# Kernel tuning notes

Hardware: AMD Instinct MI355X
Metric: run time of the kernel (lower is better)

## Reference

```python
import jax, jax.numpy as jnp
import numpy as np

V, D, N, E, H = 80000, 300, 32, 64, 4
C = D // H          # per-head out channels (concat -> D)
B, T, U, L = 32, 35, 1024, 3
VG = 50000          # last_idx_globals - last_idx_senses
NEG_SLOPE = 0.2


def setup_inputs() -> dict:
    key = jax.random.key(0)
    ks = jax.random.split(key, 16)
    s = 0.02
    inp = {
        'x_indices': jax.random.randint(ks[0], (B, T, N), 0, V),
        'edge_index': jax.random.randint(ks[1], (B, T, 2, E), 0, N),
        'X': jax.random.normal(ks[2], (V, D), jnp.float32) * s,
        'gat_W': jax.random.normal(ks[3], (D, H * C), jnp.float32) * s,
        'att_src': jax.random.normal(ks[4], (H, C), jnp.float32) * s,
        'att_dst': jax.random.normal(ks[5], (H, C), jnp.float32) * s,
        'gat_bias': jnp.zeros((H * C,), jnp.float32),
        'W_ih0': jax.random.normal(ks[6], (4 * U, 2 * D), jnp.float32) * s,
        'W_ih_rest': jax.random.normal(ks[7], (L - 1, 4 * U, U), jnp.float32) * s,
        'W_hh': jax.random.normal(ks[8], (L, 4 * U, U), jnp.float32) * s,
        'b_ih': jnp.zeros((L, 4 * U), jnp.float32),
        'b_hh': jnp.zeros((L, 4 * U), jnp.float32),
        'lin_W': jax.random.normal(ks[9], (VG, U), jnp.float32) * s,
        'lin_b': jnp.zeros((VG,), jnp.float32),
    }
    return inp


def _gat_node0(X, x_indices, edge_index, gat_W, att_src, att_dst, gat_bias):
    # Batched GATConv over G = B*T tiny subgraphs of fixed size N; dense NxN
    # attention per subgraph is used since N=32 (G*H*N*N ~ 4.6M floats).
    b, t, n = x_indices.shape
    G = b * t
    idx = x_indices.reshape(G, n)
    ei = edge_index.reshape(G, 2, -1)
    x = X[idx]                                   # [G,N,D] embedding gather
    h = (x @ gat_W).reshape(G, n, H, C)          # [G,N,H,C]
    a_s = jnp.einsum('gnhc,hc->gnh', h, att_src)
    a_d = jnp.einsum('gnhc,hc->gnh', h, att_dst)
    # e[g,h,i,j] = leaky_relu(a_dst_i + a_src_j)  (messages j -> i)
    e = a_d.transpose(0, 2, 1)[:, :, :, None] + a_s.transpose(0, 2, 1)[:, :, None, :]
    e = jax.nn.leaky_relu(e, NEG_SLOPE)
    src, dst = ei[:, 0], ei[:, 1]
    g_ar = jnp.arange(G)[:, None]
    adj = jnp.zeros((G, n, n), bool).at[g_ar, dst, src].set(True)
    diag = jnp.arange(n)
    adj = adj.at[:, diag, diag].set(True)        # PyG GATConv adds self-loops
    e = jnp.where(adj[:, None, :, :], e, jnp.float32(-1e9))
    alpha = jax.nn.softmax(e, axis=-1)           # softmax over source nodes j
    out = jnp.einsum('ghij,gjhc->gihc', alpha, h)
    node0 = out[:, 0].reshape(G, H * C) + gat_bias  # only node 0 is consumed
    return node0.reshape(b, t, H * C)


def _lstm_layer(xs, Wi, Wh, bi, bh):
    # xs: [T,B,in]; PyTorch gate order i,f,g,o
    bsz, u = xs.shape[1], Wh.shape[1]
    def step(carry, xt):
        hp, cp = carry
        g = xt @ Wi.T + hp @ Wh.T + (bi + bh)
        i_, f_, gg, o_ = jnp.split(g, 4, axis=-1)
        c = jax.nn.sigmoid(f_) * cp + jax.nn.sigmoid(i_) * jnp.tanh(gg)
        hh = jax.nn.sigmoid(o_) * jnp.tanh(c)
        return (hh, c), hh
    init = (jnp.zeros((bsz, u), xs.dtype), jnp.zeros((bsz, u), xs.dtype))
    _, ys = jax.lax.scan(step, init, xs)
    return ys


def reference(x_indices, edge_index, X, gat_W, att_src, att_dst, gat_bias,
              W_ih0, W_ih_rest, W_hh, b_ih, b_hh, lin_W, lin_b):
    b, t, n = x_indices.shape
    node0 = _gat_node0(X, x_indices, edge_index, gat_W, att_src, att_dst, gat_bias)
    curr_emb = X[x_indices[:, :, 0]]                       # [B,T,D]
    sig = jnp.concatenate([curr_emb, node0], axis=-1)      # [B,T,2D]
    seq = sig.transpose(1, 0, 2)                           # [T,B,2D]
    ys = _lstm_layer(seq, W_ih0, W_hh[0], b_ih[0], b_hh[0])
    for l in range(W_ih_rest.shape[0]):
        ys = _lstm_layer(ys, W_ih_rest[l], W_hh[l + 1], b_ih[l + 1], b_hh[l + 1])
    lstm_out = ys.transpose(1, 0, 2).reshape(b * t, -1)    # [B*T,U]
    logits = lstm_out @ lin_W.T + lin_b                    # [B*T,VG]
    return jax.nn.log_softmax(logits, axis=-1)
```

## Files before the change

### kernel.cpp

```cpp
#include <hip/hip_runtime.h>

#define DEV __device__ __forceinline__

typedef __attribute__((ext_vector_type(8))) short short8;
typedef __attribute__((ext_vector_type(4))) float f32x4;
typedef unsigned short u16;

constexpr int kV = 80000, kD = 300, kNN = 32, kEE = 64, kHH = 4, kCC = 75;
constexpr int kB = 32, kT = 35, kU = 1024, kVG = 50000;
constexpr int kG = kB * kT;
constexpr int kM = kG;

constexpr size_t alignup(size_t x) { return (x + 255) & ~size_t(255); }
constexpr size_t OFF_BAR   = 0;
constexpr size_t OFF_WSRC  = 1024;
constexpr size_t OFF_WDST  = alignup(OFF_WSRC + 1200 * 4);
constexpr size_t OFF_BIAS  = alignup(OFF_WDST + 1200 * 4);
constexpr size_t OFF_SIG   = alignup(OFF_BIAS + 3 * 4096 * 4);
constexpr size_t OFF_WX0   = alignup(OFF_SIG + (size_t)35 * 32 * 640 * 2);
constexpr size_t OFF_WX12  = alignup(OFF_WX0 + (size_t)4096 * 640 * 2);
constexpr size_t OFF_GATES = alignup(OFF_WX12 + (size_t)2 * 4096 * 1024 * 2);
constexpr size_t OFF_HIST  = alignup(OFF_GATES + (size_t)1120 * 4096 * 4);
constexpr size_t OFF_PART  = alignup(OFF_HIST + (size_t)3 * 35 * 32 * 1024 * 2);
constexpr size_t OFF_LSE   = alignup(OFF_PART + (size_t)1120 * 784 * 8);
constexpr size_t OFF_LINWB = alignup(OFF_LSE + 1120 * 4);
constexpr size_t kLinWBytes = (size_t)kVG * 1024 * 2;
constexpr size_t kNeedBW   = OFF_LINWB + kLinWBytes;
constexpr size_t OFF_WHB   = alignup(OFF_LINWB + kLinWBytes);
constexpr size_t kWhbBytes = (size_t)3 * 4096 * 1024 * 2;
constexpr size_t kNeedWHB  = OFF_WHB + kWhbBytes;

DEV u16 f2bf(float f) {
  union { float f; unsigned u; } v; v.f = f;
  unsigned r = v.u + 0x7fffu + ((v.u >> 16) & 1u);
  return (u16)(r >> 16);
}
DEV float fexp(float x) { return __builtin_amdgcn_exp2f(x * 1.4426950408889634f); }
DEV float fsigm(float x) {
  float t = __builtin_amdgcn_exp2f(-1.4426950408889634f * x);
  return __builtin_amdgcn_rcpf(1.f + t);
}
DEV float ftanh(float x) {
  float xc = fminf(fmaxf(x, -20.f), 20.f);
  float t = __builtin_amdgcn_exp2f(2.8853900817779268f * xc);
  return (t - 1.f) * __builtin_amdgcn_rcpf(t + 1.f);
}
DEV f32x4 mfma16(short8 a, short8 b, f32x4 c) {
  return __builtin_amdgcn_mfma_f32_16x16x32_bf16(a, b, c, 0, 0, 0);
}
DEV void store_u16_llc(u16* p, u16 v) {
  unsigned vv = v;
  asm volatile("global_store_short %0, %1, off sc0 sc1"
               :: "v"(p), "v"(vv) : "memory");
}
DEV void gll16(const void* g, void* l) {
  __builtin_amdgcn_global_load_lds(
      (const __attribute__((address_space(1))) unsigned int*)g,
      (__attribute__((address_space(3))) unsigned int*)l, 16, 0, 0);
}
DEV void conv_slice(const float* src, u16* dst, long n, long tid0, long stride) {
  long n8 = n >> 3;
  for (long i = tid0; i < n8; i += stride) {
    long o = i * 8;
    float4 a = *(const float4*)(src + o);
    float4 b = *(const float4*)(src + o + 4);
    u16 t[8] = {f2bf(a.x), f2bf(a.y), f2bf(a.z), f2bf(a.w),
                f2bf(b.x), f2bf(b.y), f2bf(b.z), f2bf(b.w)};
    *(uint4*)(dst + o) = *(const uint4*)t;
  }
}

__global__ void prep_small(const float* __restrict__ gat_W,
                           const float* __restrict__ att_src,
                           const float* __restrict__ att_dst,
                           const float* __restrict__ b_ih,
                           const float* __restrict__ b_hh,
                           float* __restrict__ ws_src, float* __restrict__ ws_dst,
                           float* __restrict__ bias_sum) {
  int total = 1200 + 1200 + 3 * 4096;
  for (int i = blockIdx.x * blockDim.x + threadIdx.x; i < total; i += gridDim.x * blockDim.x) {
    if (i < 1200) {
      int d = i >> 2, h = i & 3;
      float s = 0.f;
      for (int c = 0; c < kCC; ++c) s += gat_W[d * 300 + h * kCC + c] * att_src[h * kCC + c];
      ws_src[i] = s;
    } else if (i < 2400) {
      int j = i - 1200; int d = j >> 2, h = j & 3;
      float s = 0.f;
      for (int c = 0; c < kCC; ++c) s += gat_W[d * 300 + h * kCC + c] * att_dst[h * kCC + c];
      ws_dst[j] = s;
    } else {
      int j = i - 2400;
      bias_sum[j] = b_ih[j] + b_hh[j];
    }
  }
}

__global__ void wx_prep(const float* __restrict__ W_ih0,
                        const float* __restrict__ W_ih_rest,
                        const float* __restrict__ W_hh,
                        u16* __restrict__ wx0, u16* __restrict__ wx12,
                        u16* __restrict__ whb, int nhh_layers) {
  const int n0 = 4096 * 640;
  const int n12 = 2 * 4096 * 1024;
  const int nhh = nhh_layers * 4096 * 1024;
  int total = n0 + n12 + nhh;
  for (int i = blockIdx.x * blockDim.x + threadIdx.x; i < total; i += gridDim.x * blockDim.x) {
    if (i < n0) {
      int row = i / 640, col = i - row * 640;
      float v = (col < 600) ? W_ih0[row * 600 + col] : 0.f;
      wx0[i] = f2bf(v);
    } else if (i < n0 + n12) {
      int j = i - n0;
      wx12[j] = f2bf(W_ih_rest[j]);
    } else {
      int j = i - n0 - n12;
      if (whb) whb[j] = f2bf(W_hh[j]);
    }
  }
}

__global__ void wb_conv(const float* __restrict__ W, u16* __restrict__ Wb) {
  const long n = (long)kVG * 1024;
  conv_slice(W, Wb, n, (long)(blockIdx.x * blockDim.x + threadIdx.x),
             (long)gridDim.x * blockDim.x);
}

__global__ void __launch_bounds__(256) gat_kernel(
    const int* __restrict__ x_indices, const int* __restrict__ edge_index,
    const float* __restrict__ X, const float* __restrict__ gat_W,
    const float* __restrict__ gat_bias, const float* __restrict__ ws_src,
    const float* __restrict__ ws_dst, u16* __restrict__ sig) {
  __shared__ float xs[32][301];
  __shared__ float a_s[32][4];
  __shared__ float a_d0[4];
  __shared__ float alpha[4][32];
  __shared__ float xw[4][301];
  __shared__ int allowed[32];
  int g = blockIdx.x, tid = threadIdx.x;
  const int* idx = x_indices + g * 32;
  for (int i = tid; i < 32 * 300; i += 256) {
    int j = i / 300, d2 = i - j * 300;
    xs[j][d2] = X[(size_t)idx[j] * 300 + d2];
  }
  if (tid < 32) allowed[tid] = (tid == 0) ? 1 : 0;
  __syncthreads();
  if (tid < 128) {
    int j = tid >> 2, h = tid & 3;
    float s = 0.f;
    for (int d2 = 0; d2 < 300; ++d2) s += xs[j][d2] * ws_src[d2 * 4 + h];
    a_s[j][h] = s;
  } else if (tid < 132) {
    int h = tid - 128; float s = 0.f;
    for (int d2 = 0; d2 < 300; ++d2) s += xs[0][d2] * ws_dst[d2 * 4 + h];
    a_d0[h] = s;
  } else if (tid >= 192) {
    int e = tid - 192;
    int src = edge_index[g * 128 + e];
    int dst = edge_index[g * 128 + 64 + e];
    if (dst == 0) allowed[src] = 1;
  }
  __syncthreads();
  if (tid < 4) {
    int h = tid;
    float ev[32];
    float mx = -1e30f;
    #pragma unroll
    for (int j = 0; j < 32; ++j) {
      float v = a_d0[h] + a_s[j][h];
      v = (v > 0.f) ? v : 0.2f * v;
      v = allowed[j] ? v : -1e9f;
      ev[j] = v; mx = fmaxf(mx, v);
    }
    float ssum = 0.f;
    #pragma unroll
    for (int j = 0; j < 32; ++j) { float p = fexp(ev[j] - mx); ev[j] = p; ssum += p; }
    float inv = 1.f / ssum;
    #pragma unroll
    for (int j = 0; j < 32; ++j) alpha[h][j] = ev[j] * inv;
  }
  __syncthreads();
  for (int i = tid; i < 4 * 300; i += 256) {
    int h = i / 300, d2 = i - h * 300;
    float s = 0.f;
    #pragma unroll
    for (int j = 0; j < 32; ++j) s += alpha[h][j] * xs[j][d2];
    xw[h][d2] = s;
  }
  __syncthreads();
  int t = g % 35, b = g / 35;
  u16* srow = sig + ((size_t)t * 32 + b) * 640;
  for (int hc = tid; hc < 300; hc += 256) {
    srow[hc] = f2bf(xs[0][hc]);
    int h = hc / 75;
    float s = gat_bias[hc];
    for (int d2 = 0; d2 < 300; ++d2) s += xw[h][d2] * gat_W[d2 * 300 + hc];
    srow[300 + hc] = f2bf(s);
  }
  for (int i2 = 600 + tid; i2 < 640; i2 += 256) srow[i2] = 0;
}

__global__ void __launch_bounds__(256, 4) gemm_ig(
    const u16* __restrict__ A, const u16* __restrict__ Bw,
    float* __restrict__ gates, int K) {
  int bid = blockIdx.x;
  int bm = bid % 9, bn = bid / 9;
  int m0 = bm * 128, n0 = bn * 128;
  int tid = threadIdx.x, w = tid >> 6, lane = tid & 63, l15 = lane & 15, lhi = lane >> 4;
  int wm = w & 1, wn = w >> 1;
  __shared__ u16 As[2][128][32];
  __shared__ u16 Bs[2][128][32];
  int cl = ((lane & 3) ^ ((lane >> 3) & 3)) * 8;
  int am0 = m0 + w * 32 + (lane >> 2);
  int am1 = am0 + 16;
  const u16* arow0 = A + (size_t)((am0 < kM) ? am0 : 0) * K + cl;
  const u16* arow1 = A + (size_t)((am1 < kM) ? am1 : 0) * K + cl;
  int bn0r = n0 + w * 32 + (lane >> 2);
  const u16* brow0 = Bw + (size_t)bn0r * K + cl;
  const u16* brow1 = Bw + (size_t)(bn0r + 16) * K + cl;
  const int koff = (lhi ^ ((l15 >> 1) & 3)) * 8;

  f32x4 acc[4][4];
  #pragma unroll
  for (int i = 0; i < 4; ++i)
    #pragma unroll
    for (int j = 0; j < 4; ++j) { f32x4 z = {0.f, 0.f, 0.f, 0.f}; acc[i][j] = z; }

  auto ISSUE = [&](int k0, int buf) {
    gll16(arow0 + k0, &As[buf][w * 32][0]);
    gll16(arow1 + k0, &As[buf][w * 32 + 16][0]);
    gll16(brow0 + k0, &Bs[buf][w * 32][0]);
    gll16(brow1 + k0, &Bs[buf][w * 32 + 16][0]);
  };
  int nkt = K >> 5;
  ISSUE(0, 0);
  for (int kt = 0; kt < nkt; ++kt) {
    int cur = kt & 1;
    if (kt < nkt - 1) {
      ISSUE((kt + 1) * 32, cur ^ 1);
      asm volatile("s_waitcnt vmcnt(4)" ::: "memory");
    } else {
      asm volatile("s_waitcnt vmcnt(0)" ::: "memory");
    }
    __builtin_amdgcn_s_barrier();
    __builtin_amdgcn_sched_barrier(0);
    short8 bfr[4];
    #pragma unroll
    for (int nt = 0; nt < 4; ++nt)
      bfr[nt] = *(const short8*)&Bs[cur][wn * 64 + nt * 16 + l15][koff];
    #pragma unroll
    for (int mt = 0; mt < 4; ++mt) {
      short8 af = *(const short8*)&As[cur][wm * 64 + mt * 16 + l15][koff];
      #pragma unroll
      for (int nt = 0; nt < 4; ++nt)
        acc[mt][nt] = mfma16(af, bfr[nt], acc[mt][nt]);
    }
    __builtin_amdgcn_sched_barrier(0);
    __builtin_amdgcn_s_barrier();
  }
  #pragma unroll
  for (int mt = 0; mt < 4; ++mt) {
    #pragma unroll
    for (int r = 0; r < 4; ++r) {
      int m = m0 + wm * 64 + mt * 16 + lhi * 4 + r;
      if (m < kM) {
        float* orow = gates + (size_t)m * 4096;
        #pragma unroll
        for (int nt = 0; nt < 4; ++nt) {
          int n = n0 + wn * 64 + nt * 16 + l15;
          orow[(n & 1023) * 4 + (n >> 10)] = acc[mt][nt][r];
        }
      }
    }
  }
}

__global__ void __launch_bounds__(256, 1) lstm_rec(
    const float* __restrict__ W_hh_l,
    const u16* __restrict__ whb_l,
    const float* __restrict__ gates,
    const float* __restrict__ bias_l,
    u16* __restrict__ hout,
    unsigned* flags, unsigned sbase,
    const float* csrcA, u16* cdstA, long ncA,
    const float* csrcB, u16* cdstB, long ncB) {
  if (blockIdx.x >= 128) {
    long tid0 = (long)(blockIdx.x - 128) * 256 + threadIdx.x;
    long stride = 128L * 256;
    if (cdstA) conv_slice(csrcA, cdstA, ncA, tid0, stride);
    if (cdstB) conv_slice(csrcB, cdstB, ncB, tid0, stride);
    return;
  }
  const int p = blockIdx.x;
  const int tid = threadIdx.x;
  const int w = tid >> 6, lane = tid & 63, l15 = lane & 15, lhi = lane >> 4;
  __shared__ u16 whs[32][1032];
  __shared__ float pred[4][32][33];
  if (whb_l) {
    for (int i = tid; i < 32 * 128; i += 256) {
      int row = i >> 7, seg = i & 127;
      int g = row >> 3, jj = row & 7;
      uint4 v = *(const uint4*)(whb_l + (((size_t)(g * 1024 + p * 8 + jj)) << 10) + seg * 8);
      *(uint4*)&whs[row][seg * 8] = v;
    }
  } else {
    for (int i = tid; i < 32 * 256; i += 256) {
      int row = i >> 8, seg = i & 255;
      int g = row >> 3, jj = row & 7;
      const float* src = W_hh_l + (((size_t)(g * 1024 + p * 8 + jj)) << 10) + seg * 4;
      float4 f = *(const float4*)src;
      u16 tmp[4] = {f2bf(f.x), f2bf(f.y), f2bf(f.z), f2bf(f.w)};
      *(uint2*)&whs[row][seg * 4] = *(const uint2*)tmp;
    }
  }
  const int bb = tid >> 3, jj2 = tid & 7;
  float bias_r[4];
  #pragma unroll
  for (int g = 0; g < 4; ++g) bias_r[g] = bias_l[g * 1024 + p * 8 + jj2];
  float c_reg = 0.f;
  const int kbase = w * 256;
  const float4* gb4 = (const float4*)gates + (size_t)bb * 1024 + (p * 8 + jj2);
  const unsigned* myflags = flags + w * 32 + (lane & 31);

  float4 gx = gb4[0];

  for (int t = 0; t < 35; ++t) {
    float4 gxn;
    if (t > 0) {
      unsigned tgt = sbase + (unsigned)t;
      while (!__all((int)(__hip_atomic_load(myflags, __ATOMIC_RELAXED,
                                            __HIP_MEMORY_SCOPE_AGENT) >= tgt)))
        __builtin_amdgcn_s_sleep(1);
      asm volatile("" ::: "memory");
      const u16* hp = hout + (size_t)(t - 1) * 32 * 1024;
      const u16* hrow0 = hp + l15 * 1024 + lhi * 8;
      const u16* hrow1 = hp + (l15 + 16) * 1024 + lhi * 8;
      f32x4 acc00 = {0,0,0,0}, acc01 = {0,0,0,0}, acc10 = {0,0,0,0}, acc11 = {0,0,0,0};
      #pragma unroll
      for (int kk = 0; kk < 8; ++kk) {
        int k = kbase + kk * 32;
        short8 bf0 = *(const short8*)(hrow0 + k);
        short8 bf1 = *(const short8*)(hrow1 + k);
        short8 af0 = *(const short8*)&whs[l15][k + lhi * 8];
        short8 af1 = *(const short8*)&whs[16 + l15][k + lhi * 8];
        acc00 = mfma16(af0, bf0, acc00);
        acc01 = mfma16(af0, bf1, acc01);
        acc10 = mfma16(af1, bf0, acc10);
        acc11 = mfma16(af1, bf1, acc11);
      }
      if (t < 34) gxn = gb4[(size_t)(t + 1) * 32768];
      #pragma unroll
      for (int r = 0; r < 4; ++r) {
        pred[w][lhi * 4 + r][l15]       = acc00[r];
        pred[w][lhi * 4 + r][l15 + 16]  = acc01[r];
        pred[w][16 + lhi * 4 + r][l15]      = acc10[r];
        pred[w][16 + lhi * 4 + r][l15 + 16] = acc11[r];
      }
      __syncthreads();
    } else {
      gxn = gb4[(size_t)32 * 1024];
    }
    float pre[4];
    #pragma unroll
    for (int g = 0; g < 4; ++g) {
      float s = 0.f;
      if (t > 0) {
        int row = g * 8 + jj2;
        s = pred[0][row][bb] + pred[1][row][bb] + pred[2][row][bb] + pred[3][row][bb];
      }
      pre[g] = s;
    }
    float iv = gx.x + pre[0] + bias_r[0];
    float fv = gx.y + pre[1] + bias_r[1];
    float gv = gx.z + pre[2] + bias_r[2];
    float ov = gx.w + pre[3] + bias_r[3];
    float cc = fsigm(fv) * c_reg + fsigm(iv) * ftanh(gv);
    float hh = fsigm(ov) * ftanh(cc);
    c_reg = cc;
    store_u16_llc(hout + ((size_t)(t * 32 + bb)) * 1024 + p * 8 + jj2, f2bf(hh));
    __syncthreads();
    if (t < 34 && tid == 0)
      __hip_atomic_store(flags + p, sbase + (unsigned)t + 1u,
                         __ATOMIC_RELAXED, __HIP_MEMORY_SCOPE_AGENT);
    gx = gxn;
  }
}

DEV void logits_epilogue(f32x4 (&acc)[4][4], int m0, int n0, int wm, int wn,
                         int l15, int lhi, const float* lin_b,
                         float* out, float2* partials, int bn) {
  float bcol[4]; int ncol[4];
  #pragma unroll
  for (int nt = 0; nt < 4; ++nt) {
    int n = n0 + wn * 64 + nt * 16 + l15;
    ncol[nt] = n;
    bcol[nt] = (n < kVG) ? lin_b[n] : -INFINITY;
  }
  #pragma unroll
  for (int mt = 0; mt < 4; ++mt) {
    #pragma unroll
    for (int r = 0; r < 4; ++r) {
      int m = m0 + wm * 64 + mt * 16 + lhi * 4 + r;
      float v0 = acc[mt][0][r] + bcol[0];
      float v1 = acc[mt][1][r] + bcol[1];
      float v2 = acc[mt][2][r] + bcol[2];
      float v3 = acc[mt][3][r] + bcol[3];
      bool mok = (m < kM);
      if (mok) {
        float* orow = out + (size_t)m * kVG;
        if (ncol[0] < kVG) orow[ncol[0]] = v0;
        if (ncol[1] < kVG) orow[ncol[1]] = v1;
        if (ncol[2] < kVG) orow[ncol[2]] = v2;
        if (ncol[3] < kVG) orow[ncol[3]] = v3;
      }
      float mx = fmaxf(fmaxf(v0, v1), fmaxf(v2, v3));
      #pragma unroll
      for (int d2 = 1; d2 < 16; d2 <<= 1) mx = fmaxf(mx, __shfl_xor(mx, d2, 64));
      float sv = 0.f;
      sv += (v0 > -1e30f) ? fexp(v0 - mx) : 0.f;
      sv += (v1 > -1e30f) ? fexp(v1 - mx) : 0.f;
      sv += (v2 > -1e30f) ? fexp(v2 - mx) : 0.f;
      sv += (v3 > -1e30f) ? fexp(v3 - mx) : 0.f;
      #pragma unroll
      for (int d2 = 1; d2 < 16; d2 <<= 1) sv += __shfl_xor(sv, d2, 64);
      if (mok && l15 == 0)
        partials[(size_t)m * 784 + bn * 2 + wn] = make_float2(mx, sv);
    }
  }
}

__global__ void __launch_bounds__(256, 4) gemm_logits_async(
    const u16* __restrict__ hist2, const u16* __restrict__ linwb,
    const float* __restrict__ lin_b, float* __restrict__ out,
    float2* __restrict__ partials) {
  int nwg = gridDim.x, orig = blockIdx.x;
  int q = nwg >> 3, r = nwg & 7, xcd = orig & 7, off = orig >> 3;
  int bid = (xcd < r ? xcd * (q + 1) : r * (q + 1) + (xcd - r) * q) + off;
  int bm = bid % 9, bn = bid / 9;
  int m0 = bm * 128, n0 = bn * 128;
  int tid = threadIdx.x, w = tid >> 6, lane = tid & 63, l15 = lane & 15, lhi = lane >> 4;
  int wm = w & 1, wn = w >> 1;
  __shared__ u16 As[2][128][32];
  __shared__ u16 Bs[2][128][32];
  int cl = ((lane & 3) ^ ((lane >> 3) & 3)) * 8;
  int am0 = m0 + w * 32 + (lane >> 2);
  int am1 = am0 + 16;
  int mm0 = (am0 < kM) ? am0 : 0, mm1 = (am1 < kM) ? am1 : 0;
  const u16* arow0 = hist2 + (((size_t)((mm0 % 35) * 32 + mm0 / 35)) << 10) + cl;
  const u16* arow1 = hist2 + (((size_t)((mm1 % 35) * 32 + mm1 / 35)) << 10) + cl;
  int nr0 = n0 + w * 32 + (lane >> 2);
  int nn0 = (nr0 < kVG) ? nr0 : 0, nn1 = (nr0 + 16 < kVG) ? nr0 + 16 : 0;
  const u16* brow0 = linwb + ((size_t)nn0 << 10) + cl;
  const u16* brow1 = linwb + ((size_t)nn1 << 10) + cl;
  const int koff = (lhi ^ ((l15 >> 1) & 3)) * 8;

  f32x4 acc[4][4];
  #pragma unroll
  for (int i = 0; i < 4; ++i)
    #pragma unroll
    for (int j = 0; j < 4; ++j) { f32x4 z = {0.f, 0.f, 0.f, 0.f}; acc[i][j] = z; }

  auto ISSUE = [&](int k0, int buf) {
    gll16(arow0 + k0, &As[buf][w * 32][0]);
    gll16(arow1 + k0, &As[buf][w * 32 + 16][0]);
    gll16(brow0 + k0, &Bs[buf][w * 32][0]);
    gll16(brow1 + k0, &Bs[buf][w * 32 + 16][0]);
  };
  ISSUE(0, 0);
  for (int kt = 0; kt < 32; ++kt) {
    int cur = kt & 1;
    if (kt < 31) {
      ISSUE((kt + 1) * 32, cur ^ 1);
      asm volatile("s_waitcnt vmcnt(4)" ::: "memory");
    } else {
      asm volatile("s_waitcnt vmcnt(0)" ::: "memory");
    }
    __builtin_amdgcn_s_barrier();
    __builtin_amdgcn_sched_barrier(0);
    short8 bfr[4];
    #pragma unroll
    for (int nt = 0; nt < 4; ++nt)
      bfr[nt] = *(const short8*)&Bs[cur][wn * 64 + nt * 16 + l15][koff];
    #pragma unroll
    for (int mt = 0; mt < 4; ++mt) {
      short8 af = *(const short8*)&As[cur][wm * 64 + mt * 16 + l15][koff];
      #pragma unroll
      for (int nt = 0; nt < 4; ++nt)
        acc[mt][nt] = mfma16(af, bfr[nt], acc[mt][nt]);
    }
    __builtin_amdgcn_sched_barrier(0);
    __builtin_amdgcn_s_barrier();
  }
  logits_epilogue(acc, m0, n0, wm, wn, l15, lhi, lin_b, out, partials, bn);
}

__global__ void __launch_bounds__(256, 1) gemm_logits_fb(
    const u16* __restrict__ hist2, const float* __restrict__ lin_W,
    const float* __restrict__ lin_b, float* __restrict__ out,
    float2* __restrict__ partials) {
  int nwg = gridDim.x, orig = blockIdx.x;
  int q = nwg >> 3, r = nwg & 7, xcd = orig & 7, off = orig >> 3;
  int bid = (xcd < r ? xcd * (q + 1) : r * (q + 1) + (xcd - r) * q) + off;
  int bm = bid % 9, bn = bid / 9;
  int m0 = bm * 128, n0 = bn * 128;
  int tid = threadIdx.x, w = tid >> 6, lane = tid & 63, l15 = lane & 15, lhi = lane >> 4;
  int wm = w & 1, wn = w >> 1;
  __shared__ u16 As[128][40];
  __shared__ u16 Bs[128][40];
  f32x4 acc[4][4];
  #pragma unroll
  for (int i = 0; i < 4; ++i)
    #pragma unroll
    for (int j = 0; j < 4; ++j) { f32x4 z = {0.f, 0.f, 0.f, 0.f}; acc[i][j] = z; }
  for (int kt = 0; kt < 32; ++kt) {
    int k0 = kt * 32;
    #pragma unroll
    for (int q2 = 0; q2 < 2; ++q2) {
      int c = tid * 2 + q2; int row = c >> 2; int ch = c & 3;
      int m = m0 + row;
      uint4 av{0u, 0u, 0u, 0u};
      if (m < kM) {
        int b = m / 35; int t = m - b * 35;
        av = *(const uint4*)(hist2 + ((size_t)(t * 32 + b) << 10) + k0 + ch * 8);
      }
      *(uint4*)&As[row][ch * 8] = av;
      int n = n0 + row;
      uint4 bv{0u, 0u, 0u, 0u};
      if (n < kVG) {
        const float* src = lin_W + (size_t)n * 1024 + k0 + ch * 8;
        float4 f0 = *(const float4*)(src);
        float4 f1 = *(const float4*)(src + 4);
        bv.x = (unsigned)f2bf(f0.x) | ((unsigned)f2bf(f0.y) << 16);
        bv.y = (unsigned)f2bf(f0.z) | ((unsigned)f2bf(f0.w) << 16);
        bv.z = (unsigned)f2bf(f1.x) | ((unsigned)f2bf(f1.y) << 16);
        bv.w = (unsigned)f2bf(f1.z) | ((unsigned)f2bf(f1.w) << 16);
      }
      *(uint4*)&Bs[row][ch * 8] = bv;
    }
    __syncthreads();
    short8 bfr[4];
    #pragma unroll
    for (int nt = 0; nt < 4; ++nt)
      bfr[nt] = *(const short8*)&Bs[wn * 64 + nt * 16 + l15][lhi * 8];
    #pragma unroll
    for (int mt = 0; mt < 4; ++mt) {
      short8 af = *(const short8*)&As[wm * 64 + mt * 16 + l15][lhi * 8];
      #pragma unroll
      for (int nt = 0; nt < 4; ++nt)
        acc[mt][nt] = mfma16(af, bfr[nt], acc[mt][nt]);
    }
    __syncthreads();
  }
  logits_epilogue(acc, m0, n0, wm, wn, l15, lhi, lin_b, out, partials, bn);
}

__global__ void reduce_rows(const float2* __restrict__ partials, float* __restrict__ lse) {
  int m = blockIdx.x, tid = threadIdx.x;
  float mx = -INFINITY, s = 0.f;
  for (int j = tid; j < 782; j += 256) {
    float2 p = partials[(size_t)m * 784 + j];
    if (p.x > mx) { s = s * fexp(mx - p.x) + p.y; mx = p.x; }
    else          { s += p.y * fexp(p.x - mx); }
  }
  for (int d = 1; d < 64; d <<= 1) {
    float omx = __shfl_xor(mx, d, 64);
    float os  = __shfl_xor(s, d, 64);
    if (omx > mx) { s = s * fexp(mx - omx) + os; mx = omx; }
    else          { s += os * fexp(omx - mx); }
  }
  __shared__ float smx[4], ssum[4];
  int w = tid >> 6;
  if ((tid & 63) == 0) { smx[w] = mx; ssum[w] = s; }
  __syncthreads();
  if (tid == 0) {
    for (int i = 1; i < 4; ++i) {
      float omx = smx[i], os = ssum[i];
      if (omx > mx) { s = s * fexp(mx - omx) + os; mx = omx; }
      else          { s += os * fexp(omx - mx); }
    }
    lse[m] = mx + logf(s);
  }
}

__global__ void sub_lse(float* __restrict__ out, const float* __restrict__ lse) {
  const int total4 = 14000000;
  for (int i = blockIdx.x * blockDim.x + threadIdx.x; i < total4; i += gridDim.x * blockDim.x) {
    int m = i / 12500;
    float4 v = ((float4*)out)[i];
    float L = lse[m];
    v.x -= L; v.y -= L; v.z -= L; v.w -= L;
    ((float4*)out)[i] = v;
  }
}

extern "C" void kernel_launch(void* const* d_in, const int* in_sizes, int n_in,
                              void* d_out, int out_size, void* d_ws, size_t ws_size,
                              hipStream_t stream) {
  const int*   x_indices  = (const int*)d_in[0];
  const int*   edge_index = (const int*)d_in[1];
  const float* X          = (const float*)d_in[2];
  const float* gat_W      = (const float*)d_in[3];
  const float* att_src    = (const float*)d_in[4];
  const float* att_dst    = (const float*)d_in[5];
  const float* gat_bias   = (const float*)d_in[6];
  const float* W_ih0      = (const float*)d_in[7];
  const float* W_ih_rest  = (const float*)d_in[8];
  const float* W_hh       = (const float*)d_in[9];
  const float* b_ih       = (const float*)d_in[10];
  const float* b_hh       = (const float*)d_in[11];
  const float* lin_W      = (const float*)d_in[12];
  const float* lin_b      = (const float*)d_in[13];
  float* out = (float*)d_out;
  char* ws = (char*)d_ws;

  unsigned* flags    = (unsigned*)(ws + OFF_BAR);
  float*    ws_src   = (float*)(ws + OFF_WSRC);
  float*    ws_dst   = (float*)(ws + OFF_WDST);
  float*    bias_sum = (float*)(ws + OFF_BIAS);
  u16*      sig      = (u16*)(ws + OFF_SIG);
  u16*      wx0      = (u16*)(ws + OFF_WX0);
  u16*      wx12     = (u16*)(ws + OFF_WX12);
  float*    gates    = (float*)(ws + OFF_GATES);
  u16*      hist     = (u16*)(ws + OFF_HIST);
  float2*   partials = (float2*)(ws + OFF_PART);
  float*    lse      = (float*)(ws + OFF_LSE);
  u16*      linwb    = (u16*)(ws + OFF_LINWB);
  u16*      whb      = (u16*)(ws + OFF_WHB);
  bool use_bw  = (ws_size >= kNeedBW);
  bool use_whb = (ws_size >= kNeedWHB);
  bool hide = use_bw && use_whb;

  u16* hist0 = hist;
  u16* hist1 = hist + (size_t)35 * 32 * 1024;
  u16* hist2 = hist + (size_t)2 * 35 * 32 * 1024;
  const long nLinHalf = (long)kVG * 1024 / 2;

  hipMemsetAsync(ws + OFF_BAR, 0, 1024, stream);
  prep_small<<<64, 256, 0, stream>>>(gat_W, att_src, att_dst, b_ih, b_hh,
                                     ws_src, ws_dst, bias_sum);
  wx_prep<<<2048, 256, 0, stream>>>(W_ih0, W_ih_rest, W_hh, wx0, wx12,
                                    use_whb ? whb : nullptr, hide ? 1 : 3);
  if (use_bw && !hide) wb_conv<<<2048, 256, 0, stream>>>(lin_W, linwb);
  gat_kernel<<<kG, 256, 0, stream>>>(x_indices, edge_index, X, gat_W, gat_bias,
                                     ws_src, ws_dst, sig);
  gemm_ig<<<288, 256, 0, stream>>>(sig, wx0, gates, 640);
  lstm_rec<<<hide ? 256 : 128, 256, 0, stream>>>(
      W_hh, use_whb ? whb : nullptr, gates, bias_sum, hist0, flags, 0u,
      hide ? W_hh + (size_t)4096 * 1024 : nullptr,
      hide ? whb + (size_t)4096 * 1024 : nullptr, (long)2 * 4096 * 1024,
      hide ? lin_W : nullptr, hide ? linwb : nullptr, nLinHalf);
  gemm_ig<<<288, 256, 0, stream>>>(hist0, wx12, gates, 1024);
  lstm_rec<<<hide ? 256 : 128, 256, 0, stream>>>(
      W_hh + (size_t)4096 * 1024,
      use_whb ? whb + (size_t)4096 * 1024 : nullptr,
      gates, bias_sum + 4096, hist1, flags, 34u,
      hide ? lin_W + nLinHalf : nullptr,
      hide ? linwb + nLinHalf : nullptr, nLinHalf,
      nullptr, nullptr, 0);
  gemm_ig<<<288, 256, 0, stream>>>(hist1, wx12 + (size_t)4096 * 1024, gates, 1024);
  lstm_rec<<<128, 256, 0, stream>>>(
      W_hh + (size_t)2 * 4096 * 1024,
      use_whb ? whb + (size_t)2 * 4096 * 1024 : nullptr,
      gates, bias_sum + 8192, hist2, flags, 68u,
      nullptr, nullptr, 0, nullptr, nullptr, 0);
  if (use_bw)
    gemm_logits_async<<<9 * 391, 256, 0, stream>>>(hist2, linwb, lin_b, out, partials);
  else
    gemm_logits_fb<<<9 * 391, 256, 0, stream>>>(hist2, lin_W, lin_b, out, partials);
  reduce_rows<<<kG, 256, 0, stream>>>(partials, lse);
  sub_lse<<<2048, 256, 0, stream>>>(out, lse);
}
```

Measured before the change: 1.064 ms.

## Fuse LSTM layers 0 and 1 into one wavefront-pipelined recurrent kernel

Replaces the separate layer-0 recurrence, the layer-1 input GEMM and the layer-1 recurrence with one persistent kernel of 256 blocks. Each block owns 4 hidden units and runs layer 1 one timestep behind layer 0, computing layer 1's input projection on the fly from the fresh layer-0 output. This removes a kernel launch, a full GEMM pass and one serialized recurrence chain. In exchange it drops the bf16 W_hh precompute and the hidden lin_W conversion that used to run inside the recurrent kernels. Each step now does more MFMA work behind a single flag barrier across 256 blocks.

```diff
diff --git a/kernel.cpp b/kernel.cpp
--- a/kernel.cpp
+++ b/kernel.cpp
@@ -26,9 +26,6 @@
 constexpr size_t OFF_LINWB = alignup(OFF_LSE + 1120 * 4);
 constexpr size_t kLinWBytes = (size_t)kVG * 1024 * 2;
 constexpr size_t kNeedBW   = OFF_LINWB + kLinWBytes;
-constexpr size_t OFF_WHB   = alignup(OFF_LINWB + kLinWBytes);
-constexpr size_t kWhbBytes = (size_t)3 * 4096 * 1024 * 2;
-constexpr size_t kNeedWHB  = OFF_WHB + kWhbBytes;
 
 DEV u16 f2bf(float f) {
   union { float f; unsigned u; } v; v.f = f;
@@ -57,17 +54,6 @@
   __builtin_amdgcn_global_load_lds(
       (const __attribute__((address_space(1))) unsigned int*)g,
       (__attribute__((address_space(3))) unsigned int*)l, 16, 0, 0);
-}
-DEV void conv_slice(const float* src, u16* dst, long n, long tid0, long stride) {
-  long n8 = n >> 3;
-  for (long i = tid0; i < n8; i += stride) {
-    long o = i * 8;
-    float4 a = *(const float4*)(src + o);
-    float4 b = *(const float4*)(src + o + 4);
-    u16 t[8] = {f2bf(a.x), f2bf(a.y), f2bf(a.z), f2bf(a.w),
-                f2bf(b.x), f2bf(b.y), f2bf(b.z), f2bf(b.w)};
-    *(uint4*)(dst + o) = *(const uint4*)t;
-  }
 }
 
 __global__ void prep_small(const float* __restrict__ gat_W,
@@ -98,32 +84,32 @@
 
 __global__ void wx_prep(const float* __restrict__ W_ih0,
                         const float* __restrict__ W_ih_rest,
-                        const float* __restrict__ W_hh,
-                        u16* __restrict__ wx0, u16* __restrict__ wx12,
-                        u16* __restrict__ whb, int nhh_layers) {
+                        u16* __restrict__ wx0, u16* __restrict__ wx12) {
   const int n0 = 4096 * 640;
-  const int n12 = 2 * 4096 * 1024;
-  const int nhh = nhh_layers * 4096 * 1024;
-  int total = n0 + n12 + nhh;
+  const int n2 = 4096 * 1024;
+  int total = n0 + n2;
   for (int i = blockIdx.x * blockDim.x + threadIdx.x; i < total; i += gridDim.x * blockDim.x) {
     if (i < n0) {
       int row = i / 640, col = i - row * 640;
       float v = (col < 600) ? W_ih0[row * 600 + col] : 0.f;
       wx0[i] = f2bf(v);
-    } else if (i < n0 + n12) {
+    } else {
       int j = i - n0;
-      wx12[j] = f2bf(W_ih_rest[j]);
-    } else {
-      int j = i - n0 - n12;
-      if (whb) whb[j] = f2bf(W_hh[j]);
+      wx12[(size_t)4096 * 1024 + j] = f2bf(W_ih_rest[(size_t)4096 * 1024 + j]);
     }
   }
 }
 
 __global__ void wb_conv(const float* __restrict__ W, u16* __restrict__ Wb) {
   const long n = (long)kVG * 1024;
-  conv_slice(W, Wb, n, (long)(blockIdx.x * blockDim.x + threadIdx.x),
-             (long)gridDim.x * blockDim.x);
+  long stride = (long)gridDim.x * blockDim.x * 8;
+  for (long i = (long)(blockIdx.x * blockDim.x + threadIdx.x) * 8; i < n; i += stride) {
+    float4 a = *(const float4*)(W + i);
+    float4 b = *(const float4*)(W + i + 4);
+    u16 t[8] = {f2bf(a.x), f2bf(a.y), f2bf(a.z), f2bf(a.w),
+                f2bf(b.x), f2bf(b.y), f2bf(b.z), f2bf(b.w)};
+    *(uint4*)(Wb + i) = *(const uint4*)t;
+  }
 }
 
 __global__ void __launch_bounds__(256) gat_kernel(
@@ -275,43 +261,177 @@
   }
 }
 
+__global__ void __launch_bounds__(256, 1) lstm_fused01(
+    const float* __restrict__ W_hh,
+    const float* __restrict__ W_ih_rest,
+    const float* __restrict__ gates,
+    const float* __restrict__ bias_sum,
+    u16* __restrict__ hist0, u16* __restrict__ hist1,
+    unsigned* __restrict__ flags) {
+  const int p = blockIdx.x;
+  const int u0 = p * 4;
+  const int tid = threadIdx.x;
+  const int w = tid >> 6, lane = tid & 63, l15 = lane & 15, lhi = lane >> 4;
+  __shared__ u16 wh0[16][1032];
+  __shared__ u16 wh1[16][1032];
+  __shared__ u16 wi1[16][1032];
+  __shared__ float pred0[4][16][33];
+  __shared__ float pred1[4][16][33];
+
+  for (int i = tid; i < 16 * 256; i += 256) {
+    int row = i >> 8, seg = (i & 255) * 4;
+    int g = row >> 2, j = row & 3;
+    size_t grow = (size_t)(g * 1024 + u0 + j) * 1024 + seg;
+    float4 f0 = *(const float4*)(W_hh + grow);
+    u16 t0[4] = {f2bf(f0.x), f2bf(f0.y), f2bf(f0.z), f2bf(f0.w)};
+    *(uint2*)&wh0[row][seg] = *(const uint2*)t0;
+    float4 f1 = *(const float4*)(W_hh + (size_t)4096 * 1024 + grow);
+    u16 t1[4] = {f2bf(f1.x), f2bf(f1.y), f2bf(f1.z), f2bf(f1.w)};
+    *(uint2*)&wh1[row][seg] = *(const uint2*)t1;
+    float4 f2 = *(const float4*)(W_ih_rest + grow);
+    u16 t2[4] = {f2bf(f2.x), f2bf(f2.y), f2bf(f2.z), f2bf(f2.w)};
+    *(uint2*)&wi1[row][seg] = *(const uint2*)t2;
+  }
+
+  const int half = tid >> 7;
+  const int pb = (tid & 127) >> 2;
+  const int pj = tid & 3;
+  float bias_r[4];
+  #pragma unroll
+  for (int g = 0; g < 4; ++g)
+    bias_r[g] = bias_sum[half * 4096 + g * 1024 + u0 + pj];
+  float c_reg = 0.f;
+  const int kbase = w * 256;
+  const unsigned* myflag = flags + w * 64 + lane;
+  __syncthreads();
+
+  for (int s = 0; s < 36; ++s) {
+    const bool l0act = s < 35;
+    const bool l1act = s >= 1;
+    if (s >= 1) {
+      unsigned tgt = (unsigned)s;
+      while (!__all((int)(__hip_atomic_load(myflag, __ATOMIC_RELAXED,
+                                            __HIP_MEMORY_SCOPE_AGENT) >= tgt)))
+        __builtin_amdgcn_s_sleep(1);
+      asm volatile("" ::: "memory");
+    }
+    f32x4 a00 = {0,0,0,0}, a01 = {0,0,0,0};
+    f32x4 a10 = {0,0,0,0}, a11 = {0,0,0,0};
+    if (l0act && s >= 1) {
+      const u16* hp = hist0 + (size_t)(s - 1) * 32 * 1024;
+      const u16* h0p = hp + l15 * 1024 + lhi * 8;
+      const u16* h1p = hp + (l15 + 16) * 1024 + lhi * 8;
+      #pragma unroll
+      for (int kk = 0; kk < 8; ++kk) {
+        int k = kbase + kk * 32;
+        short8 af = *(const short8*)&wh0[l15][k + lhi * 8];
+        short8 b0 = *(const short8*)(h0p + k);
+        short8 b1 = *(const short8*)(h1p + k);
+        a00 = mfma16(af, b0, a00);
+        a01 = mfma16(af, b1, a01);
+      }
+    }
+    if (l1act) {
+      const u16* xp = hist0 + (size_t)(s - 1) * 32 * 1024;
+      const u16* x0p = xp + l15 * 1024 + lhi * 8;
+      const u16* x1p = xp + (l15 + 16) * 1024 + lhi * 8;
+      #pragma unroll
+      for (int kk = 0; kk < 8; ++kk) {
+        int k = kbase + kk * 32;
+        short8 af = *(const short8*)&wi1[l15][k + lhi * 8];
+        short8 b0 = *(const short8*)(x0p + k);
+        short8 b1 = *(const short8*)(x1p + k);
+        a10 = mfma16(af, b0, a10);
+        a11 = mfma16(af, b1, a11);
+      }
+      if (s >= 2) {
+        const u16* hp = hist1 + (size_t)(s - 2) * 32 * 1024;
+        const u16* h0p = hp + l15 * 1024 + lhi * 8;
+        const u16* h1p = hp + (l15 + 16) * 1024 + lhi * 8;
+        #pragma unroll
+        for (int kk = 0; kk < 8; ++kk) {
+          int k = kbase + kk * 32;
+          short8 af = *(const short8*)&wh1[l15][k + lhi * 8];
+          short8 b0 = *(const short8*)(h0p + k);
+          short8 b1 = *(const short8*)(h1p + k);
+          a10 = mfma16(af, b0, a10);
+          a11 = mfma16(af, b1, a11);
+        }
+      }
+    }
+    #pragma unroll
+    for (int r = 0; r < 4; ++r) {
+      pred0[w][lhi * 4 + r][l15]      = a00[r];
+      pred0[w][lhi * 4 + r][l15 + 16] = a01[r];
+      pred1[w][lhi * 4 + r][l15]      = a10[r];
+      pred1[w][lhi * 4 + r][l15 + 16] = a11[r];
+    }
+    __syncthreads();
+    if (half == 0) {
+      if (l0act) {
+        int t0 = s;
+        float4 gx = ((const float4*)gates)[(size_t)(t0 * 32 + pb) * 1024 + u0 + pj];
+        float pre[4];
+        #pragma unroll
+        for (int g = 0; g < 4; ++g) {
+          int row = g * 4 + pj;
+          pre[g] = pred0[0][row][pb] + pred0[1][row][pb] +
+                   pred0[2][row][pb] + pred0[3][row][pb];
+        }
+        float iv = gx.x + pre[0] + bias_r[0];
+        float fv = gx.y + pre[1] + bias_r[1];
+        float gv = gx.z + pre[2] + bias_r[2];
+        float ov = gx.w + pre[3] + bias_r[3];
+        float cc = fsigm(fv) * c_reg + fsigm(iv) * ftanh(gv);
+        float hh = fsigm(ov) * ftanh(cc);
+        c_reg = cc;
+        store_u16_llc(hist0 + ((size_t)(t0 * 32 + pb) << 10) + u0 + pj, f2bf(hh));
+      }
+    } else {
+      if (l1act) {
+        int t1 = s - 1;
+        float pre[4];
+        #pragma unroll
+        for (int g = 0; g < 4; ++g) {
+          int row = g * 4 + pj;
+          pre[g] = pred1[0][row][pb] + pred1[1][row][pb] +
+                   pred1[2][row][pb] + pred1[3][row][pb];
+        }
+        float iv = pre[0] + bias_r[0];
+        float fv = pre[1] + bias_r[1];
+        float gv = pre[2] + bias_r[2];
+        float ov = pre[3] + bias_r[3];
+        float cc = fsigm(fv) * c_reg + fsigm(iv) * ftanh(gv);
+        float hh = fsigm(ov) * ftanh(cc);
+        c_reg = cc;
+        store_u16_llc(hist1 + ((size_t)(t1 * 32 + pb) << 10) + u0 + pj, f2bf(hh));
+      }
+    }
+    __syncthreads();
+    if (s < 35 && tid == 0)
+      __hip_atomic_store(flags + p, (unsigned)(s + 1),
+                         __ATOMIC_RELAXED, __HIP_MEMORY_SCOPE_AGENT);
+  }
+}
+
 __global__ void __launch_bounds__(256, 1) lstm_rec(
     const float* __restrict__ W_hh_l,
-    const u16* __restrict__ whb_l,
     const float* __restrict__ gates,
     const float* __restrict__ bias_l,
     u16* __restrict__ hout,
-    unsigned* flags, unsigned sbase,
-    const float* csrcA, u16* cdstA, long ncA,
-    const float* csrcB, u16* cdstB, long ncB) {
-  if (blockIdx.x >= 128) {
-    long tid0 = (long)(blockIdx.x - 128) * 256 + threadIdx.x;
-    long stride = 128L * 256;
-    if (cdstA) conv_slice(csrcA, cdstA, ncA, tid0, stride);
-    if (cdstB) conv_slice(csrcB, cdstB, ncB, tid0, stride);
-    return;
-  }
+    unsigned* flags, unsigned sbase) {
   const int p = blockIdx.x;
   const int tid = threadIdx.x;
   const int w = tid >> 6, lane = tid & 63, l15 = lane & 15, lhi = lane >> 4;
   __shared__ u16 whs[32][1032];
   __shared__ float pred[4][32][33];
-  if (whb_l) {
-    for (int i = tid; i < 32 * 128; i += 256) {
-      int row = i >> 7, seg = i & 127;
-      int g = row >> 3, jj = row & 7;
-      uint4 v = *(const uint4*)(whb_l + (((size_t)(g * 1024 + p * 8 + jj)) << 10) + seg * 8);
-      *(uint4*)&whs[row][seg * 8] = v;
-    }
-  } else {
-    for (int i = tid; i < 32 * 256; i += 256) {
-      int row = i >> 8, seg = i & 255;
-      int g = row >> 3, jj = row & 7;
-      const float* src = W_hh_l + (((size_t)(g * 1024 + p * 8 + jj)) << 10) + seg * 4;
-      float4 f = *(const float4*)src;
-      u16 tmp[4] = {f2bf(f.x), f2bf(f.y), f2bf(f.z), f2bf(f.w)};
-      *(uint2*)&whs[row][seg * 4] = *(const uint2*)tmp;
-    }
+  for (int i = tid; i < 32 * 256; i += 256) {
+    int row = i >> 8, seg = i & 255;
+    int g = row >> 3, jj = row & 7;
+    const float* src = W_hh_l + (((size_t)(g * 1024 + p * 8 + jj)) << 10) + seg * 4;
+    float4 f = *(const float4*)src;
+    u16 tmp[4] = {f2bf(f.x), f2bf(f.y), f2bf(f.z), f2bf(f.w)};
+    *(uint2*)&whs[row][seg * 4] = *(const uint2*)tmp;
   }
   const int bb = tid >> 3, jj2 = tid & 7;
   float bias_r[4];
@@ -323,6 +443,7 @@
   const unsigned* myflags = flags + w * 32 + (lane & 31);
 
   float4 gx = gb4[0];
+  __syncthreads();
 
   for (int t = 0; t < 35; ++t) {
     float4 gxn;
@@ -625,44 +746,25 @@
   float2*   partials = (float2*)(ws + OFF_PART);
   float*    lse      = (float*)(ws + OFF_LSE);
   u16*      linwb    = (u16*)(ws + OFF_LINWB);
-  u16*      whb      = (u16*)(ws + OFF_WHB);
-  bool use_bw  = (ws_size >= kNeedBW);
-  bool use_whb = (ws_size >= kNeedWHB);
-  bool hide = use_bw && use_whb;
+  bool use_bw = (ws_size >= kNeedBW);
 
   u16* hist0 = hist;
   u16* hist1 = hist + (size_t)35 * 32 * 1024;
   u16* hist2 = hist + (size_t)2 * 35 * 32 * 1024;
-  const long nLinHalf = (long)kVG * 1024 / 2;
 
   hipMemsetAsync(ws + OFF_BAR, 0, 1024, stream);
   prep_small<<<64, 256, 0, stream>>>(gat_W, att_src, att_dst, b_ih, b_hh,
                                      ws_src, ws_dst, bias_sum);
-  wx_prep<<<2048, 256, 0, stream>>>(W_ih0, W_ih_rest, W_hh, wx0, wx12,
-                                    use_whb ? whb : nullptr, hide ? 1 : 3);
-  if (use_bw && !hide) wb_conv<<<2048, 256, 0, stream>>>(lin_W, linwb);
+  wx_prep<<<1024, 256, 0, stream>>>(W_ih0, W_ih_rest, wx0, wx12);
+  if (use_bw) wb_conv<<<2048, 256, 0, stream>>>(lin_W, linwb);
   gat_kernel<<<kG, 256, 0, stream>>>(x_indices, edge_index, X, gat_W, gat_bias,
                                      ws_src, ws_dst, sig);
   gemm_ig<<<288, 256, 0, stream>>>(sig, wx0, gates, 640);
-  lstm_rec<<<hide ? 256 : 128, 256, 0, stream>>>(
-      W_hh, use_whb ? whb : nullptr, gates, bias_sum, hist0, flags, 0u,
-      hide ? W_hh + (size_t)4096 * 1024 : nullptr,
-      hide ? whb + (size_t)4096 * 1024 : nullptr, (long)2 * 4096 * 1024,
-      hide ? lin_W : nullptr, hide ? linwb : nullptr, nLinHalf);
-  gemm_ig<<<288, 256, 0, stream>>>(hist0, wx12, gates, 1024);
-  lstm_rec<<<hide ? 256 : 128, 256, 0, stream>>>(
-      W_hh + (size_t)4096 * 1024,
-      use_whb ? whb + (size_t)4096 * 1024 : nullptr,
-      gates, bias_sum + 4096, hist1, flags, 34u,
-      hide ? lin_W + nLinHalf : nullptr,
-      hide ? linwb + nLinHalf : nullptr, nLinHalf,
-      nullptr, nullptr, 0);
+  lstm_fused01<<<256, 256, 0, stream>>>(W_hh, W_ih_rest, gates, bias_sum,
+                                        hist0, hist1, flags);
   gemm_ig<<<288, 256, 0, stream>>>(hist1, wx12 + (size_t)4096 * 1024, gates, 1024);
-  lstm_rec<<<128, 256, 0, stream>>>(
-      W_hh + (size_t)2 * 4096 * 1024,
-      use_whb ? whb + (size_t)2 * 4096 * 1024 : nullptr,
-      gates, bias_sum + 8192, hist2, flags, 68u,
-      nullptr, nullptr, 0, nullptr, nullptr, 0);
+  lstm_rec<<<128, 256, 0, stream>>>(W_hh + (size_t)2 * 4096 * 1024, gates,
+                                    bias_sum + 8192, hist2, flags, 64u);
   if (use_bw)
     gemm_logits_async<<<9 * 391, 256, 0, stream>>>(hist2, linwb, lin_b, out, partials);
   else
```

After: 1.065 ms. No clear change (+0.1%).
